# Kernel optimization log

Hardware: AMD Instinct MI355X
Metric: run time of the kernel (lower is better)

## Reference

```python
import jax, jax.numpy as jnp
import numpy as np

NPG = 39      # nodes per graph, from (1+8+64+9)*(39+1)=3280 = lin1 in_features
NEG_SLOPE = 0.2


def gat_conv(x, src, dst, W, a_src, a_dst, b, n):
    """PyG GATConv, heads=1, self-loops already appended to (src, dst).
    x:[N,Fin] W:[Fin,Fout] a_src/a_dst:[Fout] b:[Fout] -> [N,Fout]"""
    h = x @ W                                        # [N,Fout]
    e = jax.nn.leaky_relu(h[src] @ a_src + h[dst] @ a_dst, NEG_SLOPE)  # [E]
    m = jax.lax.stop_gradient(jax.ops.segment_max(e, dst, num_segments=n))
    w = jnp.exp(e - m[dst])
    denom = jax.ops.segment_sum(w, dst, num_segments=n)
    alpha = w / (denom[dst] + 1e-16)                 # segment softmax per target node
    out = jax.ops.segment_sum(alpha[:, None] * h[src], dst, num_segments=n)
    return out + b


def setup_inputs() -> dict:
    key = jax.random.key(0)
    ks = jax.random.split(key, 20)
    B, DEG = 4096, 8
    N = B * NPG
    E = N * DEG
    x = jax.random.normal(ks[0], (N, 1), dtype=jnp.float32)
    # block-diagonal edges: each node emits DEG edges to random nodes in SAME graph
    src = jnp.repeat(jnp.arange(N, dtype=jnp.int64), DEG)
    offs = (src // NPG) * NPG
    dst = offs + jax.random.randint(ks[1], (E,), 0, NPG, dtype=jnp.int64)
    edge_index = jnp.stack([src, dst])
    batch_vec = jnp.repeat(jnp.arange(B, dtype=jnp.int64), NPG)

    def glorot(k, shape):
        fan = shape[0] + (shape[1] if len(shape) > 1 else 1)
        s = jnp.sqrt(6.0 / fan)
        return jax.random.uniform(k, shape, jnp.float32, -s, s)

    p = {
        'W1': glorot(ks[2], (1, 8)),   'a1s': glorot(ks[3], (8,)),  'a1d': glorot(ks[4], (8,)),  'b1': jnp.zeros((8,), jnp.float32),
        'W2': glorot(ks[5], (8, 64)),  'a2s': glorot(ks[6], (64,)), 'a2d': glorot(ks[7], (64,)), 'b2': jnp.zeros((64,), jnp.float32),
        'W3': glorot(ks[8], (64, 9)),  'a3s': glorot(ks[9], (9,)),  'a3d': glorot(ks[10], (9,)), 'b3': jnp.zeros((9,), jnp.float32),
        'lW1': glorot(ks[11], (3280, 5000)), 'lb1': jnp.zeros((5000,), jnp.float32),
        'lW2': glorot(ks[12], (5000, 1024)), 'lb2': jnp.zeros((1024,), jnp.float32),
        'lW3': glorot(ks[13], (1024, 9)),    'lb3': jnp.zeros((9,), jnp.float32),
    }
    return {'x': x, 'edge_index': edge_index, 'batch_vec': batch_vec, **p}


def reference(x, edge_index, batch_vec,
              W1, a1s, a1d, b1, W2, a2s, a2d, b2, W3, a3s, a3d, b3,
              lW1, lb1, lW2, lb2, lW3, lb3):
    N = x.shape[0]
    B = N // NPG
    loops = jnp.arange(N, dtype=edge_index.dtype)
    src = jnp.concatenate([edge_index[0], loops])   # GATConv add_self_loops=True
    dst = jnp.concatenate([edge_index[1], loops])

    res = x.reshape(B, -1)                                    # [B,39]
    out0 = jax.ops.segment_max(x, batch_vec, num_segments=B)  # [B,1]

    h1 = jax.nn.relu(gat_conv(x, src, dst, W1, a1s, a1d, b1, N))   # dropout = eval no-op
    res1 = h1.reshape(B, -1)                                   # [B,312]
    out1 = jax.ops.segment_max(h1, batch_vec, num_segments=B)

    h2 = jax.nn.relu(gat_conv(h1, src, dst, W2, a2s, a2d, b2, N))
    res2 = h2.reshape(B, -1)                                   # [B,2496]
    out2 = jax.ops.segment_max(h2, batch_vec, num_segments=B)

    h3 = jax.nn.relu(gat_conv(h2, src, dst, W3, a3s, a3d, b3, N))
    res3 = h3.reshape(B, -1)                                   # [B,351]
    out3 = jax.ops.segment_max(h3, batch_vec, num_segments=B)

    f = jnp.concatenate([res, res1, res2, res3, out0, out1, out2, out3], axis=1)  # [B,3280]
    f = jax.nn.relu(f @ lW1 + lb1)
    f = jax.nn.relu(f @ lW2 + lb2)
    return f @ lW3 + lb3                                       # [B,9]
```

## Files before the change

### kernel.cpp

```cpp
#include <hip/hip_runtime.h>
#include <hip/hip_bf16.h>
#include <hip/hip_fp16.h>
#include <stdint.h>


typedef float f32x4 __attribute__((ext_vector_type(4)));
typedef short bf16x8 __attribute__((ext_vector_type(8)));
typedef _Float16 f16x8 __attribute__((ext_vector_type(8)));

__device__ __forceinline__ unsigned fenc(float f) {
  int s = __float_as_int(f);
  return s < 0 ? ~(unsigned)s : ((unsigned)s | 0x80000000u);
}
__device__ __forceinline__ float fdec(unsigned u) {
  return (u & 0x80000000u) ? __int_as_float((int)(u & 0x7fffffffu))
                           : __int_as_float(~(int)u);
}


__global__ __launch_bounds__(128) void gnn_block(
    const float* __restrict__ x,
    const int* __restrict__ esrc, const int* __restrict__ edst,
    const float* __restrict__ W1, const float* __restrict__ a1s, const float* __restrict__ a1d, const float* __restrict__ b1,
    const float* __restrict__ W2, const float* __restrict__ a2s, const float* __restrict__ a2d, const float* __restrict__ b2,
    const float* __restrict__ W3, const float* __restrict__ a3s, const float* __restrict__ a3d, const float* __restrict__ b3,
    __hip_bfloat16* __restrict__ fA)
{
  __shared__ __align__(16) float A[1720];
  __shared__ __align__(16) __half Hh2[2816];
  __shared__ __align__(16) __half h1h[320];
  __shared__ __align__(16) float HfT[400];
  __shared__ __align__(16) float sW3T[616];
  __shared__ __align__(16) float xbuf[40];
  __shared__ __align__(16) float a2buf[128];
  __shared__ float sarr[40], darr[40], den[40];
  __shared__ unsigned umax[40];
  __shared__ unsigned umx[132];
  __shared__ float a3sb[12], a3db[12], b3b[12];

  const int tid = threadIdx.x, g = blockIdx.x, w = tid >> 6, f = tid & 63;

  const int rt = g >> 7, mi = (g >> 4) & 7, lrow = g & 15;
  const size_t gbase = (size_t)rt * 52 * 8192 + (size_t)(mi * 2) * 512 + (size_t)lrow * 8;
#define COLADDR(c) (gbase + (size_t)((c) >> 6) * 8192 + (size_t)(((c) >> 5) & 1) * 512 \
                    + (size_t)(((c) >> 3) & 3) * 128 + ((c) & 7))

  for (int i = tid; i < 576; i += 128) { int k = i / 9, f3 = i - 9 * k; sW3T[f3 * 68 + k] = W3[i]; }
  a2buf[tid] = (tid < 64) ? a2s[tid] : a2d[tid - 64];
  if (tid < 9) { a3sb[tid] = a3s[tid]; a3db[tid] = a3d[tid]; b3b[tid] = b3[tid]; }
  for (int i = tid; i < 132; i += 128) umx[i] = 0u;
  for (int i = tid; i < 430; i += 128) *(f32x4*)&A[i * 4] = (f32x4){0.f, 0.f, 0.f, 0.f};
  for (int i = tid; i < 400; i += 128) HfT[i] = 0.f;
  if (tid < 40) { den[tid] = 0.f; umax[tid] = 0u; xbuf[tid] = 0.f; }

  float xv = 0.f;
  if (tid < 39) { xv = x[g * 39 + tid]; xbuf[tid] = xv; fA[COLADDR(tid)] = __float2bfloat16(xv); }

  int els[3], eld[3];
  const int eb = g * 312, nb0 = g * 39;
#pragma unroll
  for (int it = 0; it < 3; ++it) {
    int e = it * 128 + tid, ls = -1, ld = 0;
    if (e < 351) {
      if (e < 312) { ls = esrc[eb + e] - nb0; ld = edst[eb + e] - nb0; }
      else         { ls = e - 312; ld = ls; }
    }
    els[it] = ls; eld[it] = ld;
  }
  float c_s = 0.f, c_d = 0.f;
  const float w1r = W1[tid & 7], b1r = b1[tid & 7];
#pragma unroll
  for (int ff = 0; ff < 8; ++ff) { float wv = W1[ff]; c_s += wv * a1s[ff]; c_d += wv * a1d[ff]; }
  __syncthreads();

  if (tid < 39) atomicMax(&umx[0], fenc(xv));
  float ee[3];
#pragma unroll
  for (int it = 0; it < 3; ++it) {
    if (els[it] >= 0) {
      float e = xbuf[els[it]] * c_s + xbuf[eld[it]] * c_d;
      e = (e > 0.f) ? e : 0.2f * e;
      ee[it] = e;
      atomicMax(&umax[eld[it]], fenc(e));
    }
  }
  __syncthreads();
#pragma unroll
  for (int it = 0; it < 3; ++it) {
    if (els[it] >= 0) {
      float wv = __expf(ee[it] - fdec(umax[eld[it]]));
      atomicAdd(&den[eld[it]], wv);
      atomicAdd(&A[eld[it] * 44 + els[it]], wv);
    }
  }
  __syncthreads();
  if (tid < 39) {
    const float* Ar = &A[tid * 44];
    float q = 0.f;
#pragma unroll
    for (int c = 0; c < 10; ++c) {
      f32x4 a4 = *(const f32x4*)&Ar[c * 4];
      f32x4 x4 = *(const f32x4*)&xbuf[c * 4];
      q += a4.x * x4.x + a4.y * x4.y + a4.z * x4.z + a4.w * x4.w;
    }
    sarr[tid] = q * (1.f / (den[tid] + 1e-16f));
  }
  __syncthreads();
#pragma unroll
  for (int it = 0; it < 3; ++it) {
    int slot = it * 128 + tid;
    if (slot < 312) {
      int i = slot >> 3, fi = slot & 7;
      float v = fmaxf(sarr[i] * w1r + b1r, 0.f);
      h1h[slot] = __float2half(v);
      fA[COLADDR(39 + slot)] = __float2bfloat16(v);
      atomicMax(&umx[1 + fi], fenc(v));
    }
  }
  __syncthreads();

  float ht2r[40];
  {
    float w2k[8];
#pragma unroll
    for (int k = 0; k < 8; ++k) w2k[k] = W2[k * 64 + f];
#pragma unroll
    for (int i = 0; i < 39; ++i) {
      f16x8 hr = *(const f16x8*)&h1h[i * 8];
      float hv = 0.f;
#pragma unroll
      for (int k = 0; k < 8; ++k) hv += (float)hr[k] * w2k[k];
      ht2r[i] = hv;
    }
    ht2r[39] = 0.f;
#pragma unroll
    for (int i = 0; i < 39; ++i) {
      if ((i < 20) ? (w == 0) : (w == 1))
        Hh2[i * 72 + f] = __float2half(ht2r[i]);
    }
    for (int i = tid; i < 430; i += 128) *(f32x4*)&A[i * 4] = (f32x4){0.f, 0.f, 0.f, 0.f};
    if (tid < 39) { den[tid] = 0.f; umax[tid] = 0u; }
  }
  __syncthreads();
  {
    int node = f;
    if (node < 39) {
      const float* ab = a2buf + (tid & 64);
      const __half* hr = &Hh2[node * 72];
      float s = 0.f;
#pragma unroll
      for (int c = 0; c < 8; ++c) {
        f16x8 hv = *(const f16x8*)&hr[c * 8];
        f32x4 a0 = *(const f32x4*)&ab[c * 8];
        f32x4 a1 = *(const f32x4*)&ab[c * 8 + 4];
        s += (float)hv[0] * a0.x + (float)hv[1] * a0.y + (float)hv[2] * a0.z + (float)hv[3] * a0.w
           + (float)hv[4] * a1.x + (float)hv[5] * a1.y + (float)hv[6] * a1.z + (float)hv[7] * a1.w;
      }
      if (tid < 64) sarr[node] = s; else darr[node] = s;
    }
  }
  __syncthreads();
#pragma unroll
  for (int it = 0; it < 3; ++it) {
    if (els[it] >= 0) {
      float e = sarr[els[it]] + darr[eld[it]];
      e = (e > 0.f) ? e : 0.2f * e;
      ee[it] = e;
      atomicMax(&umax[eld[it]], fenc(e));
    }
  }
  __syncthreads();
#pragma unroll
  for (int it = 0; it < 3; ++it) {
    if (els[it] >= 0) {
      float wv = __expf(ee[it] - fdec(umax[eld[it]]));
      atomicAdd(&den[eld[it]], wv);
      atomicAdd(&A[eld[it] * 44 + els[it]], wv);
    }
  }
  __syncthreads();
  {
    const float b2r = b2[f];
    for (int it = 0; it < 20; ++it) {
      int i = it * 2 + w;
      if (i < 39) {
        float inv = 1.f / (den[i] + 1e-16f);
        const float* Ar = &A[i * 44];
        float acc = 0.f;
#pragma unroll
        for (int c = 0; c < 10; ++c) {
          f32x4 a4 = *(const f32x4*)&Ar[c * 4];
          acc += a4.x * ht2r[c * 4] + a4.y * ht2r[c * 4 + 1]
               + a4.z * ht2r[c * 4 + 2] + a4.w * ht2r[c * 4 + 3];
        }
        float v = fmaxf(acc * inv + b2r, 0.f);
        Hh2[i * 72 + f] = __float2half(v);
        fA[COLADDR(351 + i * 64 + f)] = __float2bfloat16(v);
        atomicMax(&umx[9 + f], fenc(v));
      }
    }
  }
  __syncthreads();

  {
#pragma unroll
    for (int it = 0; it < 3; ++it) {
      int slot = it * 128 + tid;
      if (slot < 351) {
        int i = slot / 9, f3 = slot - 9 * i;
        const __half* hr = &Hh2[i * 72];
        const float* wr = &sW3T[f3 * 68];
        float acc = 0.f;
#pragma unroll
        for (int c = 0; c < 8; ++c) {
          f16x8 hv = *(const f16x8*)&hr[c * 8];
          f32x4 w0 = *(const f32x4*)&wr[c * 8];
          f32x4 w1 = *(const f32x4*)&wr[c * 8 + 4];
          acc += (float)hv[0] * w0.x + (float)hv[1] * w0.y + (float)hv[2] * w0.z + (float)hv[3] * w0.w
               + (float)hv[4] * w1.x + (float)hv[5] * w1.y + (float)hv[6] * w1.z + (float)hv[7] * w1.w;
        }
        HfT[f3 * 44 + i] = acc;
      }
    }
    for (int i = tid; i < 430; i += 128) *(f32x4*)&A[i * 4] = (f32x4){0.f, 0.f, 0.f, 0.f};
    if (tid < 39) { den[tid] = 0.f; umax[tid] = 0u; }
  }
  __syncthreads();
  {
    int node = f;
    if (node < 39) {
      const float* av = (tid < 64) ? a3sb : a3db;
      float s = 0.f;
#pragma unroll
      for (int f3 = 0; f3 < 9; ++f3) s += HfT[f3 * 44 + node] * av[f3];
      if (tid < 64) sarr[node] = s; else darr[node] = s;
    }
  }
  __syncthreads();
#pragma unroll
  for (int it = 0; it < 3; ++it) {
    if (els[it] >= 0) {
      float e = sarr[els[it]] + darr[eld[it]];
      e = (e > 0.f) ? e : 0.2f * e;
      ee[it] = e;
      atomicMax(&umax[eld[it]], fenc(e));
    }
  }
  __syncthreads();
#pragma unroll
  for (int it = 0; it < 3; ++it) {
    if (els[it] >= 0) {
      float wv = __expf(ee[it] - fdec(umax[eld[it]]));
      atomicAdd(&den[eld[it]], wv);
      atomicAdd(&A[eld[it] * 44 + els[it]], wv);
    }
  }
  __syncthreads();
#pragma unroll
  for (int it = 0; it < 3; ++it) {
    int slot = it * 128 + tid;
    if (slot < 351) {
      int i = slot / 9, f3 = slot - 9 * i;
      float inv = 1.f / (den[i] + 1e-16f);
      const float* Ar = &A[i * 44];
      const float* Hr = &HfT[f3 * 44];
      float acc = 0.f;
#pragma unroll
      for (int c = 0; c < 10; ++c) {
        f32x4 a4 = *(const f32x4*)&Ar[c * 4];
        f32x4 h4 = *(const f32x4*)&Hr[c * 4];
        acc += a4.x * h4.x + a4.y * h4.y + a4.z * h4.z + a4.w * h4.w;
      }
      float v = fmaxf(acc * inv + b3b[f3], 0.f);
      fA[COLADDR(2847 + slot)] = __float2bfloat16(v);
      atomicMax(&umx[73 + f3], fenc(v));
    }
  }
  __syncthreads();

  if (tid < 130) {
    int c = 3198 + tid;
    float v = (tid < 82) ? fdec(umx[tid]) : 0.f;
    fA[COLADDR(c)] = __float2bfloat16(v);
  }
#undef COLADDR
}


__global__ __launch_bounds__(256) void conv_all(
    const float* __restrict__ lW1, const float* __restrict__ lW2,
    short* __restrict__ W1T, short* __restrict__ W2T)
{
  __shared__ float t[64][68];
  const int bid = blockIdx.x, tid = threadIdx.x;
  const float* W; short* WT; int ktile, ntile, K0, N0, KT;
  if (bid < 4160) { W = lW1; WT = W1T; ktile = bid % 52; ntile = bid / 52; K0 = 3280; N0 = 5000; KT = 52; }
  else { int c2 = bid - 4160; W = lW2; WT = W2T; ktile = c2 % 80; ntile = c2 / 80; K0 = 5000; N0 = 1024; KT = 80; }

  const int kb = ktile * 64, nb = ntile * 64;
  const int tx = tid & 15, ty = tid >> 4;
#pragma unroll
  for (int r = 0; r < 4; ++r) {
    int k = kb + ty + r * 16, n = nb + tx * 4;
    float4 v = make_float4(0.f, 0.f, 0.f, 0.f);
    if (k < K0 && n < N0) v = *(const float4*)&W[(size_t)k * N0 + n];
    t[ty + r * 16][tx * 4 + 0] = v.x; t[ty + r * 16][tx * 4 + 1] = v.y;
    t[ty + r * 16][tx * 4 + 2] = v.z; t[ty + r * 16][tx * 4 + 3] = v.w;
  }
  __syncthreads();
  const int nl = tid >> 2, kc0 = tid & 3;
#pragma unroll
  for (int h = 0; h < 2; ++h) {
    int kc = kc0 + h * 4;
    int n = nb + nl, k = kb + kc * 8;
    union { bf16x8 v; __hip_bfloat16 b[8]; } z;
#pragma unroll
    for (int j = 0; j < 8; ++j) z.b[j] = __float2bfloat16(t[kc * 8 + j][nl]);
    int rt = n >> 7, mi = (n >> 4) & 7, lr = n & 15;
    int kt = k >> 6, kq = (k >> 5) & 1, lc = (k >> 3) & 3;
    size_t addr = ((((size_t)rt * KT) + kt) * 16 + mi * 2 + kq) * 512 + ((size_t)lr + 16 * lc) * 8;
    *(bf16x8*)&WT[addr] = z.v;
  }
}


__device__ __forceinline__ void gld_lds16(const void* gptr, void* l) {
  typedef const __attribute__((address_space(1))) unsigned int GU;
  typedef __attribute__((address_space(3))) unsigned int LU;
  __builtin_amdgcn_global_load_lds((GU*)gptr, (LU*)l, 16, 0, 0);
}

template<int MODE>
__global__ __launch_bounds__(256) void gemm_tiled(
    const short* __restrict__ A, const short* __restrict__ B,
    const float* __restrict__ bias, int Nreal,
    void* __restrict__ Cout, int Nn, int KT, int ktPerSplit, int outKT)
{
  __shared__ __align__(16) short lA[8192];
  __shared__ __align__(16) short lB[8192];
  const int tid = threadIdx.x;
  const int w = tid >> 6, L = tid & 63;
  const int lrow = L & 15, lch = L >> 4;
  const int mt = blockIdx.y, nt = blockIdx.x;
  const int mw = (w >> 1) * 4, nw = (w & 1) * 4;
  const int kt0 = blockIdx.z * ktPerSplit, kt1 = kt0 + ktPerSplit;

  const short* Ab = A + ((size_t)mt * KT) * 8192 + (size_t)L * 8;
  const short* Bb = B + ((size_t)nt * KT) * 8192 + (size_t)L * 8;

  f32x4 acc[4][4] = {};

  for (int kt = kt0; kt < kt1; ++kt) {
    const short* Ak = Ab + (size_t)kt * 8192;
    const short* Bk = Bb + (size_t)kt * 8192;
#pragma unroll
    for (int j = 0; j < 4; ++j) {
      int st = w * 4 + j;
      gld_lds16(Ak + st * 512, &lA[st * 512]);
      gld_lds16(Bk + st * 512, &lB[st * 512]);
    }
    __syncthreads();
#pragma unroll
    for (int kk = 0; kk < 2; ++kk) {
      bf16x8 af[4], bfr[4];
#pragma unroll
      for (int i = 0; i < 4; ++i) {
        af[i]  = *(const bf16x8*)&lA[((mw + i) * 2 + kk) * 512 + L * 8];
        bfr[i] = *(const bf16x8*)&lB[((nw + i) * 2 + kk) * 512 + L * 8];
      }
#pragma unroll
      for (int i = 0; i < 4; ++i)
#pragma unroll
        for (int j = 0; j < 4; ++j)
          acc[i][j] = __builtin_amdgcn_mfma_f32_16x16x32_bf16(af[i], bfr[j], acc[i][j], 0, 0, 0);
    }
    __syncthreads();
  }

  if (MODE == 0) {
    __hip_bfloat16* C = (__hip_bfloat16*)Cout;
#pragma unroll
    for (int j = 0; j < 4; ++j) {
      int n = nt * 128 + (nw + j) * 16 + lrow;
      float bn = (n < Nreal) ? bias[n] : 0.f;
      int kt = n >> 6, kq = (n >> 5) & 1, lc2 = (n >> 3) & 3, j2 = n & 7;
#pragma unroll
      for (int i = 0; i < 4; ++i) {
        int mi = mw + i;
        size_t base = ((((size_t)mt * outKT + kt) * 16) + mi * 2 + kq) * 512
                      + (size_t)(lch * 4) * 8 + (size_t)lc2 * 128 + j2;
#pragma unroll
        for (int r = 0; r < 4; ++r)
          C[base + r * 8] = __float2bfloat16(fmaxf(acc[i][j][r] + bn, 0.f));
      }
    }
  } else {
    __half* P = (__half*)Cout + (size_t)blockIdx.z * 4096 * 1024;
#pragma unroll
    for (int j = 0; j < 4; ++j) {
      int n = nt * 128 + (nw + j) * 16 + lrow;
#pragma unroll
      for (int i = 0; i < 4; ++i)
#pragma unroll
        for (int r = 0; r < 4; ++r) {
          int m = mt * 128 + (mw + i) * 16 + lch * 4 + r;
          P[(size_t)m * Nn + n] = __float2half(acc[i][j][r]);
        }
    }
  }
}


__global__ __launch_bounds__(256) void gemm3_fused(
    const __half* __restrict__ P,
    const float* __restrict__ b2v,
    const float* __restrict__ W3,
    const float* __restrict__ b3v,
    float* __restrict__ out)
{
  __shared__ float sW3[9 * 1024];
  int tid = threadIdx.x;
  for (int i = tid; i < 9216; i += 256) { int k = i / 9, j = i - 9 * k; sW3[j * 1024 + k] = W3[i]; }
  __syncthreads();
  int row = blockIdx.x * 4 + (tid >> 6);
  int lane = tid & 63;
  const __half* p0 = P + (size_t)row * 1024;
  const size_t S = (size_t)4096 * 1024;
  float acc[9] = {0, 0, 0, 0, 0, 0, 0, 0, 0};
  for (int t = 0; t < 16; ++t) {
    int k = lane + 64 * t;
    float c = __half2float(p0[k]) + __half2float(p0[k + S])
            + __half2float(p0[k + 2 * S]) + __half2float(p0[k + 3 * S]) + b2v[k];
    c = fmaxf(c, 0.f);
#pragma unroll
    for (int j = 0; j < 9; ++j) acc[j] += c * sW3[j * 1024 + k];
  }
#pragma unroll
  for (int j = 0; j < 9; ++j) {
    float v = acc[j];
    v += __shfl_down(v, 32, 64);
    v += __shfl_down(v, 16, 64);
    v += __shfl_down(v, 8, 64);
    v += __shfl_down(v, 4, 64);
    v += __shfl_down(v, 2, 64);
    v += __shfl_down(v, 1, 64);
    if (lane == 0) out[(size_t)row * 9 + j] = v + b3v[j];
  }
}


extern "C" void kernel_launch(void* const* d_in, const int* in_sizes, int n_in,
                              void* d_out, int out_size, void* d_ws, size_t ws_size,
                              hipStream_t stream)
{
  const float* x   = (const float*)d_in[0];
  const int*   ei  = (const int*)d_in[1];
  const float* W1  = (const float*)d_in[3];
  const float* a1s = (const float*)d_in[4];
  const float* a1d = (const float*)d_in[5];
  const float* b1  = (const float*)d_in[6];
  const float* W2  = (const float*)d_in[7];
  const float* a2s = (const float*)d_in[8];
  const float* a2d = (const float*)d_in[9];
  const float* b2  = (const float*)d_in[10];
  const float* W3  = (const float*)d_in[11];
  const float* a3s = (const float*)d_in[12];
  const float* a3d = (const float*)d_in[13];
  const float* b3  = (const float*)d_in[14];
  const float* lW1 = (const float*)d_in[15];
  const float* lb1 = (const float*)d_in[16];
  const float* lW2 = (const float*)d_in[17];
  const float* lb2 = (const float*)d_in[18];
  const float* lW3 = (const float*)d_in[19];
  const float* lb3 = (const float*)d_in[20];

  const int E = 4096 * 39 * 8;
  const int* esrc = ei;
  const int* edst = ei + E;

  short* fA  = (short*)d_ws;
  short* W1T = fA  + (size_t)4096 * 3328;
  short* C1  = W1T + (size_t)5120 * 3328;
  short* W2T = C1  + (size_t)4096 * 5120;
  __half* P  = (__half*)d_ws;

  conv_all<<<5440, 256, 0, stream>>>(lW1, lW2, W1T, W2T);
  gnn_block<<<4096, 128, 0, stream>>>(x, esrc, edst,
                                      W1, a1s, a1d, b1, W2, a2s, a2d, b2, W3, a3s, a3d, b3,
                                      (__hip_bfloat16*)fA);
  gemm_tiled<0><<<dim3(40, 32, 1), 256, 0, stream>>>(fA, W1T, lb1, 5000, C1, 5120, 52, 52, 80);
  gemm_tiled<1><<<dim3(8, 32, 4), 256, 0, stream>>>(C1, W2T, nullptr, 1024, P, 1024, 80, 20, 0);
  gemm3_fused<<<1024, 256, 0, stream>>>(P, lb2, lW3, lb3, (float*)d_out);
}
```

Baseline: 482.1 us.

## Process one graph per wavefront, replacing block barriers with compiler fences

The GNN kernel now gives each 64-lane wavefront its own graph, with two graphs per 128-thread block and per-wave shared-memory buffers. Because a wavefront runs in lockstep, the many __syncthreads calls become compiler-only memory fences. Per-feature and input max reductions now use wave shuffles or per-lane register maxima instead of shared atomics. In exchange, each wave does twice the per-thread work and uses more LDS per block, and correctness depends on wavefront-synchronous execution of LDS operations.

```diff
diff --git a/kernel.cpp b/kernel.cpp
--- a/kernel.cpp
+++ b/kernel.cpp
@@ -8,6 +8,8 @@
 typedef short bf16x8 __attribute__((ext_vector_type(8)));
 typedef _Float16 f16x8 __attribute__((ext_vector_type(8)));
 
+#define CFENCE() asm volatile("" ::: "memory")
+
 __device__ __forceinline__ unsigned fenc(float f) {
   int s = __float_as_int(f);
   return s < 0 ? ~(unsigned)s : ((unsigned)s | 0x80000000u);
@@ -18,7 +20,7 @@
 }
 
 
-__global__ __launch_bounds__(128) void gnn_block(
+__global__ __launch_bounds__(128) void gnn_wave(
     const float* __restrict__ x,
     const int* __restrict__ esrc, const int* __restrict__ edst,
     const float* __restrict__ W1, const float* __restrict__ a1s, const float* __restrict__ a1d, const float* __restrict__ b1,
@@ -26,41 +28,57 @@
     const float* __restrict__ W3, const float* __restrict__ a3s, const float* __restrict__ a3d, const float* __restrict__ b3,
     __hip_bfloat16* __restrict__ fA)
 {
-  __shared__ __align__(16) float A[1720];
-  __shared__ __align__(16) __half Hh2[2816];
-  __shared__ __align__(16) __half h1h[320];
-  __shared__ __align__(16) float HfT[400];
-  __shared__ __align__(16) float sW3T[616];
-  __shared__ __align__(16) float xbuf[40];
-  __shared__ __align__(16) float a2buf[128];
-  __shared__ float sarr[40], darr[40], den[40];
-  __shared__ unsigned umax[40];
-  __shared__ unsigned umx[132];
+  __shared__ float sW3T[616];
+  __shared__ float a2buf[128];
   __shared__ float a3sb[12], a3db[12], b3b[12];
-
-  const int tid = threadIdx.x, g = blockIdx.x, w = tid >> 6, f = tid & 63;
+  __shared__ __align__(16) float AA[2][1720];
+  __shared__ __align__(16) __half Hh2A[2][2816];
+  __shared__ __align__(16) __half h1hA[2][320];
+  __shared__ __align__(16) float HfTA[2][400];
+  __shared__ __align__(16) float xbufA[2][40];
+  __shared__ float sarrA[2][40], darrA[2][40], denA[2][40];
+  __shared__ unsigned umaxA[2][40];
+  __shared__ unsigned umxA[2][132];
+
+  const int tid = threadIdx.x, w = tid >> 6, L = tid & 63;
+  const int g = blockIdx.x * 2 + w;
+
+  for (int i = tid; i < 576; i += 128) { int k = i / 9, f3 = i - 9 * k; sW3T[f3 * 68 + k] = W3[i]; }
+  a2buf[tid] = (tid < 64) ? a2s[tid] : a2d[tid - 64];
+  if (tid < 9) { a3sb[tid] = a3s[tid]; a3db[tid] = a3d[tid]; b3b[tid] = b3[tid]; }
+  __syncthreads();
+
+  float* A = AA[w];
+  __half* Hh2 = Hh2A[w];
+  __half* h1h = h1hA[w];
+  float* HfT = HfTA[w];
+  float* xbuf = xbufA[w];
+  float* sarr = sarrA[w]; float* darr = darrA[w]; float* den = denA[w];
+  unsigned* umax = umaxA[w]; unsigned* umx = umxA[w];
 
   const int rt = g >> 7, mi = (g >> 4) & 7, lrow = g & 15;
   const size_t gbase = (size_t)rt * 52 * 8192 + (size_t)(mi * 2) * 512 + (size_t)lrow * 8;
 #define COLADDR(c) (gbase + (size_t)((c) >> 6) * 8192 + (size_t)(((c) >> 5) & 1) * 512 \
                     + (size_t)(((c) >> 3) & 3) * 128 + ((c) & 7))
 
-  for (int i = tid; i < 576; i += 128) { int k = i / 9, f3 = i - 9 * k; sW3T[f3 * 68 + k] = W3[i]; }
-  a2buf[tid] = (tid < 64) ? a2s[tid] : a2d[tid - 64];
-  if (tid < 9) { a3sb[tid] = a3s[tid]; a3db[tid] = a3d[tid]; b3b[tid] = b3[tid]; }
-  for (int i = tid; i < 132; i += 128) umx[i] = 0u;
-  for (int i = tid; i < 430; i += 128) *(f32x4*)&A[i * 4] = (f32x4){0.f, 0.f, 0.f, 0.f};
-  for (int i = tid; i < 400; i += 128) HfT[i] = 0.f;
-  if (tid < 40) { den[tid] = 0.f; umax[tid] = 0u; xbuf[tid] = 0.f; }
+  for (int i = L; i < 430; i += 64) *(f32x4*)&A[i * 4] = (f32x4){0.f, 0.f, 0.f, 0.f};
+  for (int i = L; i < 400; i += 64) HfT[i] = 0.f;
+  for (int i = L; i < 132; i += 64) umx[i] = 0u;
+  if (L < 40) { den[L] = 0.f; umax[L] = 0u; xbuf[L] = 0.f; }
 
   float xv = 0.f;
-  if (tid < 39) { xv = x[g * 39 + tid]; xbuf[tid] = xv; fA[COLADDR(tid)] = __float2bfloat16(xv); }
-
-  int els[3], eld[3];
+  if (L < 39) { xv = x[g * 39 + L]; xbuf[L] = xv; fA[COLADDR(L)] = __float2bfloat16(xv); }
+  {
+    float m = (L < 39) ? xv : -1e30f;
+    for (int o = 32; o >= 1; o >>= 1) m = fmaxf(m, __shfl_xor(m, o, 64));
+    if (L == 0) umx[0] = fenc(m);
+  }
+
+  int els[6], eld[6];
   const int eb = g * 312, nb0 = g * 39;
 #pragma unroll
-  for (int it = 0; it < 3; ++it) {
-    int e = it * 128 + tid, ls = -1, ld = 0;
+  for (int it = 0; it < 6; ++it) {
+    int e = it * 64 + L, ls = -1, ld = 0;
     if (e < 351) {
       if (e < 312) { ls = esrc[eb + e] - nb0; ld = edst[eb + e] - nb0; }
       else         { ls = e - 312; ld = ls; }
@@ -68,15 +86,14 @@
     els[it] = ls; eld[it] = ld;
   }
   float c_s = 0.f, c_d = 0.f;
-  const float w1r = W1[tid & 7], b1r = b1[tid & 7];
+  const float w1r = W1[L & 7], b1r = b1[L & 7];
 #pragma unroll
   for (int ff = 0; ff < 8; ++ff) { float wv = W1[ff]; c_s += wv * a1s[ff]; c_d += wv * a1d[ff]; }
-  __syncthreads();
-
-  if (tid < 39) atomicMax(&umx[0], fenc(xv));
-  float ee[3];
-#pragma unroll
-  for (int it = 0; it < 3; ++it) {
+  CFENCE();
+
+  float ee[6];
+#pragma unroll
+  for (int it = 0; it < 6; ++it) {
     if (els[it] >= 0) {
       float e = xbuf[els[it]] * c_s + xbuf[eld[it]] * c_d;
       e = (e > 0.f) ? e : 0.2f * e;
@@ -84,18 +101,18 @@
       atomicMax(&umax[eld[it]], fenc(e));
     }
   }
-  __syncthreads();
-#pragma unroll
-  for (int it = 0; it < 3; ++it) {
+  CFENCE();
+#pragma unroll
+  for (int it = 0; it < 6; ++it) {
     if (els[it] >= 0) {
       float wv = __expf(ee[it] - fdec(umax[eld[it]]));
       atomicAdd(&den[eld[it]], wv);
       atomicAdd(&A[eld[it] * 44 + els[it]], wv);
     }
   }
-  __syncthreads();
-  if (tid < 39) {
-    const float* Ar = &A[tid * 44];
+  CFENCE();
+  if (L < 39) {
+    const float* Ar = &A[L * 44];
     float q = 0.f;
 #pragma unroll
     for (int c = 0; c < 10; ++c) {
@@ -103,12 +120,12 @@
       f32x4 x4 = *(const f32x4*)&xbuf[c * 4];
       q += a4.x * x4.x + a4.y * x4.y + a4.z * x4.z + a4.w * x4.w;
     }
-    sarr[tid] = q * (1.f / (den[tid] + 1e-16f));
-  }
-  __syncthreads();
-#pragma unroll
-  for (int it = 0; it < 3; ++it) {
-    int slot = it * 128 + tid;
+    sarr[L] = q * (1.f / (den[L] + 1e-16f));
+  }
+  CFENCE();
+#pragma unroll
+  for (int it = 0; it < 5; ++it) {
+    int slot = it * 64 + L;
     if (slot < 312) {
       int i = slot >> 3, fi = slot & 7;
       float v = fmaxf(sarr[i] * w1r + b1r, 0.f);
@@ -117,13 +134,13 @@
       atomicMax(&umx[1 + fi], fenc(v));
     }
   }
-  __syncthreads();
+  CFENCE();
 
   float ht2r[40];
   {
     float w2k[8];
 #pragma unroll
-    for (int k = 0; k < 8; ++k) w2k[k] = W2[k * 64 + f];
+    for (int k = 0; k < 8; ++k) w2k[k] = W2[k * 64 + L];
 #pragma unroll
     for (int i = 0; i < 39; ++i) {
       f16x8 hr = *(const f16x8*)&h1h[i * 8];
@@ -131,37 +148,33 @@
 #pragma unroll
       for (int k = 0; k < 8; ++k) hv += (float)hr[k] * w2k[k];
       ht2r[i] = hv;
+      Hh2[i * 72 + L] = __float2half(hv);
     }
     ht2r[39] = 0.f;
-#pragma unroll
-    for (int i = 0; i < 39; ++i) {
-      if ((i < 20) ? (w == 0) : (w == 1))
-        Hh2[i * 72 + f] = __float2half(ht2r[i]);
-    }
-    for (int i = tid; i < 430; i += 128) *(f32x4*)&A[i * 4] = (f32x4){0.f, 0.f, 0.f, 0.f};
-    if (tid < 39) { den[tid] = 0.f; umax[tid] = 0u; }
-  }
-  __syncthreads();
-  {
-    int node = f;
-    if (node < 39) {
-      const float* ab = a2buf + (tid & 64);
-      const __half* hr = &Hh2[node * 72];
-      float s = 0.f;
-#pragma unroll
-      for (int c = 0; c < 8; ++c) {
-        f16x8 hv = *(const f16x8*)&hr[c * 8];
-        f32x4 a0 = *(const f32x4*)&ab[c * 8];
-        f32x4 a1 = *(const f32x4*)&ab[c * 8 + 4];
-        s += (float)hv[0] * a0.x + (float)hv[1] * a0.y + (float)hv[2] * a0.z + (float)hv[3] * a0.w
-           + (float)hv[4] * a1.x + (float)hv[5] * a1.y + (float)hv[6] * a1.z + (float)hv[7] * a1.w;
-      }
-      if (tid < 64) sarr[node] = s; else darr[node] = s;
-    }
-  }
-  __syncthreads();
-#pragma unroll
-  for (int it = 0; it < 3; ++it) {
+    for (int i = L; i < 430; i += 64) *(f32x4*)&A[i * 4] = (f32x4){0.f, 0.f, 0.f, 0.f};
+    if (L < 39) { den[L] = 0.f; umax[L] = 0u; }
+  }
+  CFENCE();
+  if (L < 39) {
+    const __half* hr = &Hh2[L * 72];
+    float s = 0.f, d = 0.f;
+#pragma unroll
+    for (int c = 0; c < 8; ++c) {
+      f16x8 hv = *(const f16x8*)&hr[c * 8];
+      f32x4 s0 = *(const f32x4*)&a2buf[c * 8];
+      f32x4 s1 = *(const f32x4*)&a2buf[c * 8 + 4];
+      f32x4 d0 = *(const f32x4*)&a2buf[64 + c * 8];
+      f32x4 d1 = *(const f32x4*)&a2buf[64 + c * 8 + 4];
+      s += (float)hv[0] * s0.x + (float)hv[1] * s0.y + (float)hv[2] * s0.z + (float)hv[3] * s0.w
+         + (float)hv[4] * s1.x + (float)hv[5] * s1.y + (float)hv[6] * s1.z + (float)hv[7] * s1.w;
+      d += (float)hv[0] * d0.x + (float)hv[1] * d0.y + (float)hv[2] * d0.z + (float)hv[3] * d0.w
+         + (float)hv[4] * d1.x + (float)hv[5] * d1.y + (float)hv[6] * d1.z + (float)hv[7] * d1.w;
+    }
+    sarr[L] = s; darr[L] = d;
+  }
+  CFENCE();
+#pragma unroll
+  for (int it = 0; it < 6; ++it) {
     if (els[it] >= 0) {
       float e = sarr[els[it]] + darr[eld[it]];
       e = (e > 0.f) ? e : 0.2f * e;
@@ -169,43 +182,42 @@
       atomicMax(&umax[eld[it]], fenc(e));
     }
   }
-  __syncthreads();
-#pragma unroll
-  for (int it = 0; it < 3; ++it) {
+  CFENCE();
+#pragma unroll
+  for (int it = 0; it < 6; ++it) {
     if (els[it] >= 0) {
       float wv = __expf(ee[it] - fdec(umax[eld[it]]));
       atomicAdd(&den[eld[it]], wv);
       atomicAdd(&A[eld[it] * 44 + els[it]], wv);
     }
   }
-  __syncthreads();
+  CFENCE();
   {
-    const float b2r = b2[f];
-    for (int it = 0; it < 20; ++it) {
-      int i = it * 2 + w;
-      if (i < 39) {
-        float inv = 1.f / (den[i] + 1e-16f);
-        const float* Ar = &A[i * 44];
-        float acc = 0.f;
-#pragma unroll
-        for (int c = 0; c < 10; ++c) {
-          f32x4 a4 = *(const f32x4*)&Ar[c * 4];
-          acc += a4.x * ht2r[c * 4] + a4.y * ht2r[c * 4 + 1]
-               + a4.z * ht2r[c * 4 + 2] + a4.w * ht2r[c * 4 + 3];
-        }
-        float v = fmaxf(acc * inv + b2r, 0.f);
-        Hh2[i * 72 + f] = __float2half(v);
-        fA[COLADDR(351 + i * 64 + f)] = __float2bfloat16(v);
-        atomicMax(&umx[9 + f], fenc(v));
+    const float b2r = b2[L];
+    float m2 = -1e30f;
+    for (int i = 0; i < 39; ++i) {
+      float inv = 1.f / (den[i] + 1e-16f);
+      const float* Ar = &A[i * 44];
+      float acc = 0.f;
+#pragma unroll
+      for (int c = 0; c < 10; ++c) {
+        f32x4 a4 = *(const f32x4*)&Ar[c * 4];
+        acc += a4.x * ht2r[c * 4] + a4.y * ht2r[c * 4 + 1]
+             + a4.z * ht2r[c * 4 + 2] + a4.w * ht2r[c * 4 + 3];
       }
-    }
-  }
-  __syncthreads();
+      float v = fmaxf(acc * inv + b2r, 0.f);
+      Hh2[i * 72 + L] = __float2half(v);
+      fA[COLADDR(351 + i * 64 + L)] = __float2bfloat16(v);
+      m2 = fmaxf(m2, v);
+    }
+    umx[9 + L] = fenc(m2);
+  }
+  CFENCE();
 
   {
 #pragma unroll
-    for (int it = 0; it < 3; ++it) {
-      int slot = it * 128 + tid;
+    for (int it = 0; it < 6; ++it) {
+      int slot = it * 64 + L;
       if (slot < 351) {
         int i = slot / 9, f3 = slot - 9 * i;
         const __half* hr = &Hh2[i * 72];
@@ -222,23 +234,22 @@
         HfT[f3 * 44 + i] = acc;
       }
     }
-    for (int i = tid; i < 430; i += 128) *(f32x4*)&A[i * 4] = (f32x4){0.f, 0.f, 0.f, 0.f};
-    if (tid < 39) { den[tid] = 0.f; umax[tid] = 0u; }
-  }
-  __syncthreads();
-  {
-    int node = f;
-    if (node < 39) {
-      const float* av = (tid < 64) ? a3sb : a3db;
-      float s = 0.f;
-#pragma unroll
-      for (int f3 = 0; f3 < 9; ++f3) s += HfT[f3 * 44 + node] * av[f3];
-      if (tid < 64) sarr[node] = s; else darr[node] = s;
-    }
-  }
-  __syncthreads();
-#pragma unroll
-  for (int it = 0; it < 3; ++it) {
+    for (int i = L; i < 430; i += 64) *(f32x4*)&A[i * 4] = (f32x4){0.f, 0.f, 0.f, 0.f};
+    if (L < 39) { den[L] = 0.f; umax[L] = 0u; }
+  }
+  CFENCE();
+  if (L < 39) {
+    float s = 0.f, d = 0.f;
+#pragma unroll
+    for (int f3 = 0; f3 < 9; ++f3) {
+      float h = HfT[f3 * 44 + L];
+      s += h * a3sb[f3]; d += h * a3db[f3];
+    }
+    sarr[L] = s; darr[L] = d;
+  }
+  CFENCE();
+#pragma unroll
+  for (int it = 0; it < 6; ++it) {
     if (els[it] >= 0) {
       float e = sarr[els[it]] + darr[eld[it]];
       e = (e > 0.f) ? e : 0.2f * e;
@@ -246,19 +257,19 @@
       atomicMax(&umax[eld[it]], fenc(e));
     }
   }
-  __syncthreads();
-#pragma unroll
-  for (int it = 0; it < 3; ++it) {
+  CFENCE();
+#pragma unroll
+  for (int it = 0; it < 6; ++it) {
     if (els[it] >= 0) {
       float wv = __expf(ee[it] - fdec(umax[eld[it]]));
       atomicAdd(&den[eld[it]], wv);
       atomicAdd(&A[eld[it] * 44 + els[it]], wv);
     }
   }
-  __syncthreads();
-#pragma unroll
-  for (int it = 0; it < 3; ++it) {
-    int slot = it * 128 + tid;
+  CFENCE();
+#pragma unroll
+  for (int it = 0; it < 6; ++it) {
+    int slot = it * 64 + L;
     if (slot < 351) {
       int i = slot / 9, f3 = slot - 9 * i;
       float inv = 1.f / (den[i] + 1e-16f);
@@ -276,12 +287,15 @@
       atomicMax(&umx[73 + f3], fenc(v));
     }
   }
-  __syncthreads();
-
-  if (tid < 130) {
-    int c = 3198 + tid;
-    float v = (tid < 82) ? fdec(umx[tid]) : 0.f;
-    fA[COLADDR(c)] = __float2bfloat16(v);
+  CFENCE();
+
+#pragma unroll
+  for (int it = 0; it < 3; ++it) {
+    int c = 3198 + it * 64 + L;
+    if (c < 3328) {
+      float v = (c < 3280) ? fdec(umx[c - 3198]) : 0.f;
+      fA[COLADDR(c)] = __float2bfloat16(v);
+    }
   }
 #undef COLADDR
 }
@@ -485,9 +499,9 @@
   __half* P  = (__half*)d_ws;
 
   conv_all<<<5440, 256, 0, stream>>>(lW1, lW2, W1T, W2T);
-  gnn_block<<<4096, 128, 0, stream>>>(x, esrc, edst,
-                                      W1, a1s, a1d, b1, W2, a2s, a2d, b2, W3, a3s, a3d, b3,
-                                      (__hip_bfloat16*)fA);
+  gnn_wave<<<2048, 128, 0, stream>>>(x, esrc, edst,
+                                     W1, a1s, a1d, b1, W2, a2s, a2d, b2, W3, a3s, a3d, b3,
+                                     (__hip_bfloat16*)fA);
   gemm_tiled<0><<<dim3(40, 32, 1), 256, 0, stream>>>(fA, W1T, lb1, 5000, C1, 5120, 52, 52, 80);
   gemm_tiled<1><<<dim3(8, 32, 4), 256, 0, stream>>>(C1, W2T, nullptr, 1024, P, 1024, 80, 20, 0);
   gemm3_fused<<<1024, 256, 0, stream>>>(P, lb2, lW3, lb3, (float*)d_out);
```

New measurement: 474.1 us. No clear change (-1.6%).
